# Kernel optimization log

Measured on AMD Instinct MI355X. Metric: run time of the kernel, lower is better.

The kernel has to match this reference:

```python
import jax, jax.numpy as jnp
import numpy as np

B, SEQ, D, H, E = 4, 4096, 1024, 4096, 8
CAPACITY = 2.0  # k = int(S * capacity) token-expert slots


def setup_inputs() -> dict:
    key = jax.random.key(0)
    ks = jax.random.split(key, 5)
    x = jax.random.normal(ks[0], (B, SEQ, D), dtype=jnp.float32)
    gate_weight = jax.random.normal(ks[1], (E, D), dtype=jnp.float32) * 0.006
    expert_bias = jnp.ones((E, 1), dtype=jnp.float32)
    W1 = jax.random.normal(ks[2], (E, D, H), dtype=jnp.float32) * 0.02
    b1 = jnp.zeros((E, H), dtype=jnp.float32)
    W2 = jax.random.normal(ks[3], (E, H, D), dtype=jnp.float32) * 0.02
    b2 = jnp.zeros((E, D), dtype=jnp.float32)
    return {"x": x, "gate_weight": gate_weight, "expert_bias": expert_bias,
            "W1": W1, "b1": b1, "W2": W2, "b2": b2}


def reference(x, gate_weight, expert_bias, W1, b1, W2, b2):
    Bv, s, Dv = x.shape
    xf = x.reshape(-1, Dv)               # [S, D]
    S = xf.shape[0]
    k = int(S * CAPACITY)

    # router: bias_sigmoid -> scores[e, s] = sigmoid(x @ gate.T + bias)
    logits = jnp.einsum('sd,ed->es', xf, gate_weight) + expert_bias  # [E, S]
    scores = jax.nn.sigmoid(logits)

    # global top-k over flattened (E*S) token-expert pairs
    value, index = jax.lax.top_k(scores.reshape(-1), k)
    index_expert = index // S
    index_token = index % S

    # combine weights: gating score at selected slots, 0 elsewhere (topk indices unique)
    C = jnp.zeros((E * S,), dtype=scores.dtype).at[index].set(value).reshape(E, S)

    token_each_expert = jax.ops.segment_sum(
        jnp.ones((k,), dtype=jnp.float32), index_expert, num_segments=E) / float(k)

    # per-expert MLP, gated combine (tokens with C==0 contribute exactly 0,
    # matching the torch gather/MLP/index_add_ path)
    out = jnp.zeros_like(xf)
    for e in range(E):
        h = jax.nn.gelu(xf @ W1[e] + b1[e], approximate=True)  # [S, H]
        y = h @ W2[e] + b2[e]                                  # [S, D]
        out = out + C[e][:, None] * y

    x_out = out.reshape(Bv, s, Dv)
    return x_out, token_each_expert, jnp.ones((E,), dtype=scores.dtype)
```

## Files before the change

### kernel.cpp

```cpp
#include <hip/hip_runtime.h>
#include <hip/hip_bf16.h>
#include <cstdint>
#include <cstdio>
#include <math.h>

#define S_TOK 16384
#define E_EXP 8
#define DDIM  1024
#define HDIM  4096
#define K_SEL 32768
#define ES    131072
#define OUT_XO 16777216

#define WS_META    0x000000u
#define WS_HIST    0x000100u
#define WS_COUNTS  0x001100u
#define WS_EXOFF   0x001200u
#define WS_TIEIDX  0x001300u
#define WS_CLEAR   0x00A000u
#define WS_TOK     0x010000u
#define WS_COEF    0x090000u
#define WS_SCORES  0x110000u
#define WS_TCNT    0x190000u
#define WS_TSLOT   0x1A0000u
#define WS_XB      0x400000u
#define WS_W1T    0x2400000u
#define WS_W2T    0x6400000u
#define WS_HBUF   0xA400000u
#define WS_TOTAL  0x1A400000u
#define WS_YBUF   WS_W1T

typedef __attribute__((ext_vector_type(4))) float f32x4;
typedef __attribute__((ext_vector_type(8))) short bf16x8;

__device__ __forceinline__ void gload_lds16(const void* g, void* l) {
  __builtin_amdgcn_global_load_lds((const __attribute__((address_space(1))) void*)g,
                                   (__attribute__((address_space(3))) void*)l, 16, 0, 0);
}

__device__ __forceinline__ float gelu_f(float x) {
  float u = __builtin_fmaf(x * x * x, 0.044715f, x);
  float e = __builtin_amdgcn_exp2f(-2.302207976f * u);
  return x * __builtin_amdgcn_rcpf(1.0f + e);
}

#define ABUF0 0
#define ABUF1 32768
#define BBUF0 65536
#define BBUF1 98304
#define HALF  16384

#define PH_BAR() __builtin_amdgcn_s_barrier()
#define SB0()    __builtin_amdgcn_sched_barrier(0)
#define LGK0()   do { asm volatile("s_waitcnt lgkmcnt(0)"); __builtin_amdgcn_sched_barrier(0); } while (0)
#define VMC6()   asm volatile("s_waitcnt vmcnt(6)")
#define VMC0()   asm volatile("s_waitcnt vmcnt(0)")

#define GLA(DSTOFF, KE, H) do { \
  gload_lds16(aS##H##0 + (KE), lds + (DSTOFF) + w * 2048); \
  gload_lds16(aS##H##1 + (KE), lds + (DSTOFF) + w * 2048 + 1024); } while (0)
#define GLB(DSTOFF, KE, H) do { \
  gload_lds16(bS##H##0 + (KE), lds + (DSTOFF) + w * 2048); \
  gload_lds16(bS##H##1 + (KE), lds + (DSTOFF) + w * 2048 + 1024); } while (0)

#define LOAD_A(AB, ILO) do { _Pragma("unroll") for (int ii = 0; ii < 4; ii++) { \
  aF[ii][0] = *(const bf16x8*)(lds + (AB) + arow + ((ILO) + ii) * 2048 + pc0); \
  aF[ii][1] = *(const bf16x8*)(lds + (AB) + arow + ((ILO) + ii) * 2048 + pc1); } } while (0)
#define LOAD_B(BB) do { _Pragma("unroll") for (int jj = 0; jj < 4; jj++) { \
  bF[jj][0] = *(const bf16x8*)(lds + (BB) + brow + jj * 2048 + pc0); \
  bF[jj][1] = *(const bf16x8*)(lds + (BB) + brow + jj * 2048 + pc1); } } while (0)

#define MFMA_Q(ILO, JLO) do { _Pragma("unroll") for (int ii = 0; ii < 4; ii++) \
  _Pragma("unroll") for (int jj = 0; jj < 2; jj++) { \
    acc[(ILO)+ii][(JLO)+jj] = __builtin_amdgcn_mfma_f32_16x16x32_bf16(aF[ii][0], bF[(JLO)+jj][0], acc[(ILO)+ii][(JLO)+jj], 0, 0, 0); \
    acc[(ILO)+ii][(JLO)+jj] = __builtin_amdgcn_mfma_f32_16x16x32_bf16(aF[ii][1], bF[(JLO)+jj][1], acc[(ILO)+ii][(JLO)+jj], 0, 0, 0); } } while (0)

#define KGROUP(K0, AB, BB, AO, P0STG, STG, ENDWAIT) do { \
  LOAD_A(AB, 0); LOAD_B(BB); \
  if (P0STG) { GLA((AO) + HALF, (K0) + 64, 1); } \
  PH_BAR(); LGK0(); \
  __builtin_amdgcn_s_setprio(1); MFMA_Q(0, 0); __builtin_amdgcn_s_setprio(0); \
  PH_BAR(); SB0(); \
  if (STG) { GLB((BB), (K0) + 128, 0); } \
  PH_BAR(); LGK0(); \
  __builtin_amdgcn_s_setprio(1); MFMA_Q(0, 2); __builtin_amdgcn_s_setprio(0); \
  PH_BAR(); SB0(); \
  LOAD_A(AB, 4); \
  if (STG) { GLB((BB) + HALF, (K0) + 128, 1); } \
  PH_BAR(); LGK0(); \
  __builtin_amdgcn_s_setprio(1); MFMA_Q(4, 2); __builtin_amdgcn_s_setprio(0); \
  PH_BAR(); SB0(); \
  if (STG) { GLA((AB), (K0) + 128, 0); } \
  PH_BAR(); LGK0(); \
  __builtin_amdgcn_s_setprio(1); MFMA_Q(4, 0); __builtin_amdgcn_s_setprio(0); \
  ENDWAIT; \
  PH_BAR(); SB0(); \
} while (0)

__global__ __launch_bounds__(256) void transpose_bf16_kernel(
    const float* __restrict__ in, __hip_bfloat16* __restrict__ outp, int R, int C)
{
  __shared__ float tile[32][33];
  const int c0 = blockIdx.x * 32, r0 = blockIdx.y * 32;
  const size_t eoff = (size_t)blockIdx.z * (size_t)R * (size_t)C;
  const float* ip = in + eoff;
  __hip_bfloat16* op = outp + eoff;
  const int tx = threadIdx.x, ty = threadIdx.y;
#pragma unroll
  for (int i = 0; i < 4; i++) {
    int r = ty + i * 8;
    tile[r][tx] = ip[(size_t)(r0 + r) * C + c0 + tx];
  }
  __syncthreads();
#pragma unroll
  for (int i = 0; i < 4; i++) {
    int c = ty + i * 8;
    op[(size_t)(c0 + c) * R + r0 + tx] = __float2bfloat16(tile[tx][c]);
  }
}

__global__ __launch_bounds__(256) void router_kernel(
    const float* __restrict__ x, const float* __restrict__ gw, const float* __restrict__ bias,
    float* __restrict__ scores, __hip_bfloat16* __restrict__ xb)
{
  __shared__ float g[E_EXP * DDIM];
  __shared__ float bs[E_EXP];
  const int tid = threadIdx.x;
  for (int i = tid; i < E_EXP * DDIM; i += 256) g[i] = gw[i];
  if (tid < E_EXP) bs[tid] = bias[tid];
  __syncthreads();
  const int w = tid >> 6, lane = tid & 63;
  const int s = blockIdx.x * 4 + w;
  double acc[E_EXP] = {0, 0, 0, 0, 0, 0, 0, 0};
  const float* xrow = x + (size_t)s * DDIM;
  __hip_bfloat16* xbrow = xb + (size_t)s * DDIM;
#pragma unroll 4
  for (int j = 0; j < 16; j++) {
    int d = lane + 64 * j;
    float xv = xrow[d];
    xbrow[d] = __float2bfloat16(xv);
#pragma unroll
    for (int e = 0; e < E_EXP; e++) acc[e] += (double)xv * (double)g[e * DDIM + d];
  }
#pragma unroll
  for (int e = 0; e < E_EXP; e++) {
    double a = acc[e];
#pragma unroll
    for (int off = 32; off > 0; off >>= 1) a += __shfl_xor(a, off);
    acc[e] = a;
  }
  if (lane == 0) {
#pragma unroll
    for (int e = 0; e < E_EXP; e++) {
      double lg = acc[e] + (double)bs[e];
      float sc = (float)(1.0 / (1.0 + exp(-lg)));
      scores[(size_t)e * S_TOK + s] = sc;
    }
  }
}

__global__ __launch_bounds__(256) void hist_pass_kernel(
    const float* __restrict__ scores, const unsigned* __restrict__ meta,
    unsigned* __restrict__ hist, int pass)
{
  __shared__ unsigned h[256];
  const int tid = threadIdx.x;
  h[tid] = 0;
  __syncthreads();
  const unsigned prefix = meta[0];
  const int pshift = 32 - 8 * pass;
  const int bshift = 24 - 8 * pass;
  const unsigned base = blockIdx.x * 2048 + tid;
#pragma unroll
  for (int i = 0; i < 8; i++) {
    unsigned b = __float_as_uint(scores[base + i * 256]);
    bool ok = (pass == 0) || ((b >> pshift) == prefix);
    if (ok) atomicAdd(&h[(b >> bshift) & 0xFFu], 1u);
  }
  __syncthreads();
  if (h[tid]) atomicAdd(&hist[tid], h[tid]);
}

__global__ __launch_bounds__(256) void scan_pass_kernel(
    const unsigned* __restrict__ hist, unsigned* __restrict__ meta, int final)
{
  const int t = threadIdx.x;
  const unsigned v = hist[t];
  const unsigned prefix = meta[0];
  const unsigned above = meta[1];
  __shared__ unsigned csum[256];
  csum[t] = v;
  __syncthreads();
  for (int off = 1; off < 256; off <<= 1) {
    unsigned add = (t + off < 256) ? csum[t + off] : 0u;
    __syncthreads();
    csum[t] += add;
    __syncthreads();
  }
  const unsigned cge = csum[t];
  const unsigned cgt = cge - v;
  if (above + cgt < K_SEL && above + cge >= K_SEL) {
    meta[0] = (prefix << 8) | (unsigned)t;
    meta[1] = above + cgt;
    if (final) {
      meta[2] = (prefix << 8) | (unsigned)t;
      meta[4] = K_SEL - (above + cgt);
    }
  }
}

__global__ __launch_bounds__(256) void sel_kernel(const float* __restrict__ scores,
                                                  unsigned* __restrict__ meta,
                                                  unsigned* __restrict__ counts,
                                                  int* __restrict__ tok_list,
                                                  float* __restrict__ coef_list,
                                                  unsigned* __restrict__ tie_idx,
                                                  unsigned* __restrict__ tcnt,
                                                  unsigned* __restrict__ tslot)
{
  __shared__ unsigned lcnt[E_EXP], lbase[E_EXP];
  const int tid = threadIdx.x;
  if (tid < E_EXP) lcnt[tid] = 0;
  __syncthreads();
  const unsigned i = blockIdx.x * 256 + tid;
  const float v = scores[i];
  const unsigned b = __float_as_uint(v);
  const unsigned t = meta[2];
  const bool sel = (b > t);
  const unsigned e = i >> 14;
  unsigned myslot = 0;
  if (sel) myslot = atomicAdd(&lcnt[e], 1u);
  else if (b == t) {
    unsigned ts = atomicAdd(&meta[5], 1u);
    if (ts < 8192u) tie_idx[ts] = i;
  }
  __syncthreads();
  if (tid < E_EXP) lbase[tid] = atomicAdd(&counts[tid], lcnt[tid]);
  __syncthreads();
  if (sel) {
    const unsigned slot = lbase[e] + myslot;
    const unsigned p = e * S_TOK + slot;
    const unsigned tok = i & 16383u;
    tok_list[p] = (int)tok;
    coef_list[p] = v;
    unsigned us = atomicAdd(&tcnt[tok], 1u);
    tslot[tok * 8u + us] = (e << 14) | slot;
  }
}

__global__ __launch_bounds__(256) void fin_kernel(const unsigned* __restrict__ meta,
                                                  const unsigned* __restrict__ tie_idx,
                                                  unsigned* __restrict__ counts,
                                                  int* __restrict__ tok_list,
                                                  float* __restrict__ coef_list,
                                                  unsigned* __restrict__ tcnt,
                                                  unsigned* __restrict__ tslot)
{
  unsigned tcnt_ties = meta[5]; if (tcnt_ties > 8192u) tcnt_ties = 8192u;
  const unsigned q = meta[4];
  const float tval = __uint_as_float(meta[2]);
  for (unsigned t = threadIdx.x; t < tcnt_ties; t += 256) {
    unsigned idx = tie_idx[t];
    unsigned rank = 0;
    for (unsigned u = 0; u < tcnt_ties; u++) rank += (tie_idx[u] < idx) ? 1u : 0u;
    if (rank < q) {
      const unsigned e = idx >> 14;
      const unsigned tok = idx & 16383u;
      const unsigned slot = atomicAdd(&counts[e], 1u);
      tok_list[e * S_TOK + slot] = (int)tok;
      coef_list[e * S_TOK + slot] = tval;
      unsigned us = atomicAdd(&tcnt[tok], 1u);
      tslot[tok * 8u + us] = (e << 14) | slot;
    }
  }
}

__global__ void tail_kernel(const unsigned* __restrict__ counts, unsigned* __restrict__ exoff,
                            float* __restrict__ tail)
{
  if (threadIdx.x == 0) {
    unsigned o = 0;
    for (int e = 0; e < E_EXP; e++) { exoff[e] = o; o += counts[e]; }
    exoff[E_EXP] = o;
  }
  if (threadIdx.x < E_EXP) {
    tail[threadIdx.x] = (float)counts[threadIdx.x] * (1.0f / (float)K_SEL);
    tail[E_EXP + threadIdx.x] = 1.0f;
  }
}

__global__ __launch_bounds__(512, 1) void gemm1_kernel(
    const __hip_bfloat16* __restrict__ xb,
    const __hip_bfloat16* __restrict__ w1t,
    const float* __restrict__ b1,
    const int* __restrict__ tok_list,
    const unsigned* __restrict__ counts,
    const unsigned* __restrict__ exoff,
    __hip_bfloat16* __restrict__ hbuf)
{
  const int e = blockIdx.z;
  const int cnt = (int)counts[e];
  const int m0 = blockIdx.y * 256;
  if (m0 >= cnt) return;
  const int n0 = blockIdx.x * 256;

  __shared__ __align__(16) char lds[131072];
  __shared__ int s_tok[256];

  const int tid = threadIdx.x;
  const int w = tid >> 6, lane = tid & 63;
  const int wm = w >> 2, wn = w & 3;

  if (tid < 256) {
    int mi = m0 + tid;
    s_tok[tid] = tok_list[e * S_TOK + (mi < cnt ? mi : cnt - 1)];
  }
  __syncthreads();

  const int srl0 = w * 16 + (lane >> 3);
  const int srl1 = srl0 + 8;
  const int gch = ((lane & 7) ^ (lane >> 3)) * 8;
  const __hip_bfloat16* aS00 = xb + (size_t)s_tok[srl0] * DDIM + gch;
  const __hip_bfloat16* aS01 = xb + (size_t)s_tok[srl1] * DDIM + gch;
  const __hip_bfloat16* aS10 = xb + (size_t)s_tok[128 + srl0] * DDIM + gch;
  const __hip_bfloat16* aS11 = xb + (size_t)s_tok[128 + srl1] * DDIM + gch;
  const __hip_bfloat16* w1e = w1t + (size_t)e * HDIM * DDIM;
  const __hip_bfloat16* bS00 = w1e + (size_t)(n0 + srl0) * DDIM + gch;
  const __hip_bfloat16* bS01 = w1e + (size_t)(n0 + srl1) * DDIM + gch;
  const __hip_bfloat16* bS10 = w1e + (size_t)(n0 + 128 + srl0) * DDIM + gch;
  const __hip_bfloat16* bS11 = w1e + (size_t)(n0 + 128 + srl1) * DDIM + gch;

  const int arow = (wm * 128 + (lane & 15)) * 128;
  const int brow = (wn * 64 + (lane & 15)) * 128;
  const int pc0 = (((lane >> 4)) ^ (lane & 7)) * 16;
  const int pc1 = (((lane >> 4) + 4) ^ (lane & 7)) * 16;

  f32x4 acc[8][4] = {};
  bf16x8 aF[4][2], bF[4][2];

  GLA(ABUF0, 0, 0); GLA(ABUF0 + HALF, 0, 1);
  GLB(BBUF0, 0, 0); GLB(BBUF0 + HALF, 0, 1);
  GLB(BBUF1, 64, 0); GLB(BBUF1 + HALF, 64, 1);
  GLA(ABUF1, 64, 0);
  VMC6(); PH_BAR(); SB0();

  const int NKT = DDIM / 64;
  int kt = 0;
  for (; kt + 2 < NKT; kt += 2) {
    KGROUP(kt * 64, ABUF0, BBUF0, ABUF1, true, true, VMC6());
    KGROUP((kt + 1) * 64, ABUF1, BBUF1, ABUF0, true, true, VMC6());
  }
  KGROUP(kt * 64, ABUF0, BBUF0, ABUF1, true, false, VMC0());
  KGROUP((kt + 1) * 64, ABUF1, BBUF1, ABUF0, false, false, );
  VMC0();
  __syncthreads();

  __hip_bfloat16* stg = (__hip_bfloat16*)lds;
  const float* b1e = b1 + (size_t)e * HDIM;
  float bvj[4];
#pragma unroll
  for (int j = 0; j < 4; j++) bvj[j] = b1e[n0 + wn * 64 + j * 16 + (lane & 15)];
  const int pbase = (int)exoff[e] + m0;

#pragma unroll
  for (int P = 0; P < 4; P++) {
    __syncthreads();
    if (wm == (P >> 1)) {
      const int ib = (P & 1) * 4;
#pragma unroll
      for (int ii = 0; ii < 4; ii++)
#pragma unroll
        for (int jj = 0; jj < 4; jj++)
#pragma unroll
          for (int r = 0; r < 4; r++) {
            const int rloc = ii * 16 + (lane >> 4) * 4 + r;
            const int col = wn * 64 + jj * 16 + (lane & 15);
            stg[rloc * 264 + col] = __float2bfloat16(gelu_f(acc[ib + ii][jj][r] + bvj[jj]));
          }
    }
    __syncthreads();
    const int rr = tid >> 3;
    const int m = P * 64 + rr;
    if (m0 + m < cnt) {
      __hip_bfloat16* dst = hbuf + (size_t)(pbase + m) * HDIM + n0;
      const __hip_bfloat16* src = stg + rr * 264;
#pragma unroll
      for (int c = 0; c < 4; c++)
        *(uint4*)(dst + (tid & 7) * 8 + c * 64) = *(const uint4*)(src + (tid & 7) * 8 + c * 64);
    }
  }
}

__global__ __launch_bounds__(512, 1) void gemm2_kernel(
    const __hip_bfloat16* __restrict__ hbuf,
    const __hip_bfloat16* __restrict__ w2t,
    const float* __restrict__ b2,
    const float* __restrict__ coef_list,
    const unsigned* __restrict__ counts,
    const unsigned* __restrict__ exoff,
    __hip_bfloat16* __restrict__ ybuf)
{
  const int e = blockIdx.z;
  const int cnt = (int)counts[e];
  const int m0 = blockIdx.y * 256;
  if (m0 >= cnt) return;
  const int n0 = blockIdx.x * 256;

  __shared__ __align__(16) char lds[131072];
  __shared__ float s_coef[256];

  const int tid = threadIdx.x;
  const int w = tid >> 6, lane = tid & 63;
  const int wm = w >> 2, wn = w & 3;
  const int pb = (int)exoff[e];

  if (tid < 256) {
    int mi = m0 + tid;
    s_coef[tid] = (mi < cnt) ? coef_list[e * S_TOK + mi] : 0.0f;
  }
  __syncthreads();

  const int srl0 = w * 16 + (lane >> 3);
  const int srl1 = srl0 + 8;
  const int gch = ((lane & 7) ^ (lane >> 3)) * 8;
  const int ra0 = pb + ((m0 + srl0 < cnt) ? m0 + srl0 : cnt - 1);
  const int ra1 = pb + ((m0 + srl1 < cnt) ? m0 + srl1 : cnt - 1);
  const int ra2 = pb + ((m0 + 128 + srl0 < cnt) ? m0 + 128 + srl0 : cnt - 1);
  const int ra3 = pb + ((m0 + 128 + srl1 < cnt) ? m0 + 128 + srl1 : cnt - 1);
  const __hip_bfloat16* aS00 = hbuf + (size_t)ra0 * HDIM + gch;
  const __hip_bfloat16* aS01 = hbuf + (size_t)ra1 * HDIM + gch;
  const __hip_bfloat16* aS10 = hbuf + (size_t)ra2 * HDIM + gch;
  const __hip_bfloat16* aS11 = hbuf + (size_t)ra3 * HDIM + gch;
  const __hip_bfloat16* w2e = w2t + (size_t)e * DDIM * HDIM;
  const __hip_bfloat16* bS00 = w2e + (size_t)(n0 + srl0) * HDIM + gch;
  const __hip_bfloat16* bS01 = w2e + (size_t)(n0 + srl1) * HDIM + gch;
  const __hip_bfloat16* bS10 = w2e + (size_t)(n0 + 128 + srl0) * HDIM + gch;
  const __hip_bfloat16* bS11 = w2e + (size_t)(n0 + 128 + srl1) * HDIM + gch;

  const int arow = (wm * 128 + (lane & 15)) * 128;
  const int brow = (wn * 64 + (lane & 15)) * 128;
  const int pc0 = (((lane >> 4)) ^ (lane & 7)) * 16;
  const int pc1 = (((lane >> 4) + 4) ^ (lane & 7)) * 16;

  f32x4 acc[8][4] = {};
  bf16x8 aF[4][2], bF[4][2];

  GLA(ABUF0, 0, 0); GLA(ABUF0 + HALF, 0, 1);
  GLB(BBUF0, 0, 0); GLB(BBUF0 + HALF, 0, 1);
  GLB(BBUF1, 64, 0); GLB(BBUF1 + HALF, 64, 1);
  GLA(ABUF1, 64, 0);
  VMC6(); PH_BAR(); SB0();

  const int NKT = HDIM / 64;
  int kt = 0;
  for (; kt + 2 < NKT; kt += 2) {
    KGROUP(kt * 64, ABUF0, BBUF0, ABUF1, true, true, VMC6());
    KGROUP((kt + 1) * 64, ABUF1, BBUF1, ABUF0, true, true, VMC6());
  }
  KGROUP(kt * 64, ABUF0, BBUF0, ABUF1, true, false, VMC0());
  KGROUP((kt + 1) * 64, ABUF1, BBUF1, ABUF0, false, false, );
  VMC0();
  __syncthreads();

  __hip_bfloat16* stg = (__hip_bfloat16*)lds;
  const float* b2e = b2 + (size_t)e * DDIM;
  float bvj[4];
#pragma unroll
  for (int j = 0; j < 4; j++) bvj[j] = b2e[n0 + wn * 64 + j * 16 + (lane & 15)];
  const int pbase = pb + m0;

#pragma unroll
  for (int P = 0; P < 4; P++) {
    __syncthreads();
    if (wm == (P >> 1)) {
      const int ib = (P & 1) * 4;
#pragma unroll
      for (int ii = 0; ii < 4; ii++)
#pragma unroll
        for (int jj = 0; jj < 4; jj++)
#pragma unroll
          for (int r = 0; r < 4; r++) {
            const int rloc = ii * 16 + (lane >> 4) * 4 + r;
            const int col = wn * 64 + jj * 16 + (lane & 15);
            const float cf = s_coef[P * 64 + rloc];
            stg[rloc * 264 + col] = __float2bfloat16(cf * (acc[ib + ii][jj][r] + bvj[jj]));
          }
    }
    __syncthreads();
    const int rr = tid >> 3;
    const int m = P * 64 + rr;
    if (m0 + m < cnt) {
      __hip_bfloat16* dst = ybuf + (size_t)(pbase + m) * DDIM + n0;
      const __hip_bfloat16* src = stg + rr * 264;
#pragma unroll
      for (int c = 0; c < 4; c++)
        *(uint4*)(dst + (tid & 7) * 8 + c * 64) = *(const uint4*)(src + (tid & 7) * 8 + c * 64);
    }
  }
}

__global__ __launch_bounds__(256) void combine_kernel(
    const __hip_bfloat16* __restrict__ ybuf,
    const unsigned* __restrict__ tcnt,
    const unsigned* __restrict__ tslot,
    const unsigned* __restrict__ exoff,
    float* __restrict__ out)
{
  const int tid = threadIdx.x;
  const int t = blockIdx.x * 2 + (tid >> 7);
  const int d0 = (tid & 127) * 8;
  float a[8] = {0, 0, 0, 0, 0, 0, 0, 0};
  const unsigned n = tcnt[t];
  for (unsigned s = 0; s < n; s++) {
    const unsigned code = tslot[t * 8u + s];
    const unsigned p = exoff[code >> 14] + (code & 16383u);
    bf16x8 v = *(const bf16x8*)(ybuf + (size_t)p * DDIM + d0);
#pragma unroll
    for (int k = 0; k < 8; k++)
      a[k] += __uint_as_float(((unsigned)(unsigned short)v[k]) << 16);
  }
  float* op = out + (size_t)t * DDIM + d0;
  *(float4*)op = make_float4(a[0], a[1], a[2], a[3]);
  *(float4*)(op + 4) = make_float4(a[4], a[5], a[6], a[7]);
}

extern "C" void kernel_launch(void* const* d_in, const int* in_sizes, int n_in,
                              void* d_out, int out_size, void* d_ws, size_t ws_size,
                              hipStream_t stream) {
  const float* x    = (const float*)d_in[0];
  const float* gw   = (const float*)d_in[1];
  const float* bias = (const float*)d_in[2];
  const float* W1   = (const float*)d_in[3];
  const float* b1   = (const float*)d_in[4];
  const float* W2   = (const float*)d_in[5];
  const float* b2   = (const float*)d_in[6];
  float* out = (float*)d_out;
  char* ws = (char*)d_ws;

  if (ws_size < (size_t)WS_TOTAL) {
    fprintf(stderr, "kernel_launch: ws_size %zu < required %u\n", ws_size, WS_TOTAL);
    return;
  }

  unsigned* meta   = (unsigned*)(ws + WS_META);
  unsigned* hist   = (unsigned*)(ws + WS_HIST);
  unsigned* counts = (unsigned*)(ws + WS_COUNTS);
  unsigned* exoff  = (unsigned*)(ws + WS_EXOFF);
  unsigned* tiei   = (unsigned*)(ws + WS_TIEIDX);
  unsigned* tcnt   = (unsigned*)(ws + WS_TCNT);
  unsigned* tslot  = (unsigned*)(ws + WS_TSLOT);
  int*      tokl   = (int*)(ws + WS_TOK);
  float*    coefl  = (float*)(ws + WS_COEF);
  float*    scores = (float*)(ws + WS_SCORES);
  __hip_bfloat16* xb   = (__hip_bfloat16*)(ws + WS_XB);
  __hip_bfloat16* w1t  = (__hip_bfloat16*)(ws + WS_W1T);
  __hip_bfloat16* w2t  = (__hip_bfloat16*)(ws + WS_W2T);
  __hip_bfloat16* hbuf = (__hip_bfloat16*)(ws + WS_HBUF);
  __hip_bfloat16* ybuf = (__hip_bfloat16*)(ws + WS_YBUF);

  hipMemsetAsync(ws, 0, WS_CLEAR, stream);
  hipMemsetAsync(ws + WS_TCNT, 0, S_TOK * sizeof(unsigned), stream);

  transpose_bf16_kernel<<<dim3(HDIM / 32, DDIM / 32, E_EXP), dim3(32, 8), 0, stream>>>(W1, w1t, DDIM, HDIM);
  transpose_bf16_kernel<<<dim3(DDIM / 32, HDIM / 32, E_EXP), dim3(32, 8), 0, stream>>>(W2, w2t, HDIM, DDIM);

  router_kernel<<<S_TOK / 4, 256, 0, stream>>>(x, gw, bias, scores, xb);

  for (int p = 0; p < 4; p++) {
    hist_pass_kernel<<<ES / 2048, 256, 0, stream>>>(scores, meta, hist + p * 256, p);
    scan_pass_kernel<<<1, 256, 0, stream>>>(hist + p * 256, meta, p == 3);
  }
  sel_kernel<<<ES / 256, 256, 0, stream>>>(scores, meta, counts, tokl, coefl, tiei, tcnt, tslot);
  fin_kernel<<<1, 256, 0, stream>>>(meta, tiei, counts, tokl, coefl, tcnt, tslot);
  tail_kernel<<<1, 64, 0, stream>>>(counts, exoff, out + OUT_XO);

  gemm1_kernel<<<dim3(HDIM / 256, S_TOK / 256, E_EXP), 512, 0, stream>>>(
      xb, w1t, b1, tokl, counts, exoff, hbuf);
  gemm2_kernel<<<dim3(DDIM / 256, S_TOK / 256, E_EXP), 512, 0, stream>>>(
      hbuf, w2t, b2, coefl, counts, exoff, ybuf);
  combine_kernel<<<S_TOK / 2, 256, 0, stream>>>(ybuf, tcnt, tslot, exoff, out);
}
```

Measured before the change: 954.7 us.

## Restructure GEMM main loop into two-phase tiles with register-prefetched B fragments

Replaces the four-phase KGROUP schedule, which had many barriers and lgkmcnt waits, with a two-barrier-per-tile schedule in both expert GEMM kernels. A fragments are split into a03/a47 halves and B fragments into b01/b23 halves. The next tile's B fragments are read from LDS while the current MFMAs run, and global-to-LDS staging for A and B is issued at whole-tile granularity. The aim is fewer barriers and better overlap of LDS reads with MFMA work. In exchange, each tile now waits for vmcnt(0) instead of leaving loads in flight, and register pressure rises.

```diff
diff --git a/kernel.cpp b/kernel.cpp
--- a/kernel.cpp
+++ b/kernel.cpp
@@ -51,50 +51,59 @@
 #define HALF  16384
 
 #define PH_BAR() __builtin_amdgcn_s_barrier()
-#define SB0()    __builtin_amdgcn_sched_barrier(0)
-#define LGK0()   do { asm volatile("s_waitcnt lgkmcnt(0)"); __builtin_amdgcn_sched_barrier(0); } while (0)
-#define VMC6()   asm volatile("s_waitcnt vmcnt(6)")
-#define VMC0()   asm volatile("s_waitcnt vmcnt(0)")
-
-#define GLA(DSTOFF, KE, H) do { \
-  gload_lds16(aS##H##0 + (KE), lds + (DSTOFF) + w * 2048); \
-  gload_lds16(aS##H##1 + (KE), lds + (DSTOFF) + w * 2048 + 1024); } while (0)
-#define GLB(DSTOFF, KE, H) do { \
-  gload_lds16(bS##H##0 + (KE), lds + (DSTOFF) + w * 2048); \
-  gload_lds16(bS##H##1 + (KE), lds + (DSTOFF) + w * 2048 + 1024); } while (0)
-
-#define LOAD_A(AB, ILO) do { _Pragma("unroll") for (int ii = 0; ii < 4; ii++) { \
-  aF[ii][0] = *(const bf16x8*)(lds + (AB) + arow + ((ILO) + ii) * 2048 + pc0); \
-  aF[ii][1] = *(const bf16x8*)(lds + (AB) + arow + ((ILO) + ii) * 2048 + pc1); } } while (0)
-#define LOAD_B(BB) do { _Pragma("unroll") for (int jj = 0; jj < 4; jj++) { \
-  bF[jj][0] = *(const bf16x8*)(lds + (BB) + brow + jj * 2048 + pc0); \
-  bF[jj][1] = *(const bf16x8*)(lds + (BB) + brow + jj * 2048 + pc1); } } while (0)
-
-#define MFMA_Q(ILO, JLO) do { _Pragma("unroll") for (int ii = 0; ii < 4; ii++) \
+#define VMC0M()  asm volatile("s_waitcnt vmcnt(0)" ::: "memory")
+
+#define STAGE_A(DST, KE) do { \
+  gload_lds16(aS00 + (KE), lds + (DST) + w * 2048); \
+  gload_lds16(aS01 + (KE), lds + (DST) + w * 2048 + 1024); \
+  gload_lds16(aS10 + (KE), lds + (DST) + HALF + w * 2048); \
+  gload_lds16(aS11 + (KE), lds + (DST) + HALF + w * 2048 + 1024); } while (0)
+#define STAGE_B(DST, KE) do { \
+  gload_lds16(bS00 + (KE), lds + (DST) + w * 2048); \
+  gload_lds16(bS01 + (KE), lds + (DST) + w * 2048 + 1024); \
+  gload_lds16(bS10 + (KE), lds + (DST) + HALF + w * 2048); \
+  gload_lds16(bS11 + (KE), lds + (DST) + HALF + w * 2048 + 1024); } while (0)
+
+#define LDS_A03(AB) { _Pragma("unroll") for (int ii = 0; ii < 4; ii++) { \
+  a03[ii][0] = *(const bf16x8*)(lds + (AB) + arow + ii * 2048 + pc0); \
+  a03[ii][1] = *(const bf16x8*)(lds + (AB) + arow + ii * 2048 + pc1); } }
+#define LDS_A47(AB) { _Pragma("unroll") for (int ii = 0; ii < 4; ii++) { \
+  a47[ii][0] = *(const bf16x8*)(lds + (AB) + arow + (4 + ii) * 2048 + pc0); \
+  a47[ii][1] = *(const bf16x8*)(lds + (AB) + arow + (4 + ii) * 2048 + pc1); } }
+#define LDS_B01(BB) { _Pragma("unroll") for (int jj = 0; jj < 2; jj++) { \
+  b01[jj][0] = *(const bf16x8*)(lds + (BB) + brow + jj * 2048 + pc0); \
+  b01[jj][1] = *(const bf16x8*)(lds + (BB) + brow + jj * 2048 + pc1); } }
+#define LDS_B23(BB) { _Pragma("unroll") for (int jj = 0; jj < 2; jj++) { \
+  b23[jj][0] = *(const bf16x8*)(lds + (BB) + brow + (2 + jj) * 2048 + pc0); \
+  b23[jj][1] = *(const bf16x8*)(lds + (BB) + brow + (2 + jj) * 2048 + pc1); } }
+
+#define MF(AA, BF, IL, JL) { _Pragma("unroll") for (int ii = 0; ii < 4; ii++) \
   _Pragma("unroll") for (int jj = 0; jj < 2; jj++) { \
-    acc[(ILO)+ii][(JLO)+jj] = __builtin_amdgcn_mfma_f32_16x16x32_bf16(aF[ii][0], bF[(JLO)+jj][0], acc[(ILO)+ii][(JLO)+jj], 0, 0, 0); \
-    acc[(ILO)+ii][(JLO)+jj] = __builtin_amdgcn_mfma_f32_16x16x32_bf16(aF[ii][1], bF[(JLO)+jj][1], acc[(ILO)+ii][(JLO)+jj], 0, 0, 0); } } while (0)
-
-#define KGROUP(K0, AB, BB, AO, P0STG, STG, ENDWAIT) do { \
-  LOAD_A(AB, 0); LOAD_B(BB); \
-  if (P0STG) { GLA((AO) + HALF, (K0) + 64, 1); } \
-  PH_BAR(); LGK0(); \
-  __builtin_amdgcn_s_setprio(1); MFMA_Q(0, 0); __builtin_amdgcn_s_setprio(0); \
-  PH_BAR(); SB0(); \
-  if (STG) { GLB((BB), (K0) + 128, 0); } \
-  PH_BAR(); LGK0(); \
-  __builtin_amdgcn_s_setprio(1); MFMA_Q(0, 2); __builtin_amdgcn_s_setprio(0); \
-  PH_BAR(); SB0(); \
-  LOAD_A(AB, 4); \
-  if (STG) { GLB((BB) + HALF, (K0) + 128, 1); } \
-  PH_BAR(); LGK0(); \
-  __builtin_amdgcn_s_setprio(1); MFMA_Q(4, 2); __builtin_amdgcn_s_setprio(0); \
-  PH_BAR(); SB0(); \
-  if (STG) { GLA((AB), (K0) + 128, 0); } \
-  PH_BAR(); LGK0(); \
-  __builtin_amdgcn_s_setprio(1); MFMA_Q(4, 0); __builtin_amdgcn_s_setprio(0); \
-  ENDWAIT; \
-  PH_BAR(); SB0(); \
+    acc[(IL)+ii][(JL)+jj] = __builtin_amdgcn_mfma_f32_16x16x32_bf16(AA[ii][0], BF[jj][0], acc[(IL)+ii][(JL)+jj], 0, 0, 0); \
+    acc[(IL)+ii][(JL)+jj] = __builtin_amdgcn_mfma_f32_16x16x32_bf16(AA[ii][1], BF[jj][1], acc[(IL)+ii][(JL)+jj], 0, 0, 0); } }
+
+#define TILE(T, AB, BB, ABn, BBn, STGA, STGB) do { \
+  PH_BAR(); \
+  LDS_A03(AB); \
+  if (STGA) STAGE_A(ABn, ((T) + 1) * 64); \
+  __builtin_amdgcn_s_setprio(1); MF(a03, b01, 0, 0); MF(a03, b23, 0, 2); __builtin_amdgcn_s_setprio(0); \
+  VMC0M(); \
+  PH_BAR(); \
+  LDS_A47(AB); \
+  if (STGB) STAGE_B(BB, ((T) + 2) * 64); \
+  __builtin_amdgcn_s_setprio(1); MF(a47, b01, 4, 0); __builtin_amdgcn_s_setprio(0); \
+  LDS_B01(BBn); \
+  __builtin_amdgcn_s_setprio(1); MF(a47, b23, 4, 2); __builtin_amdgcn_s_setprio(0); \
+  LDS_B23(BBn); \
+} while (0)
+
+#define TILE_LAST(AB, BB) do { \
+  PH_BAR(); \
+  LDS_A03(AB); \
+  __builtin_amdgcn_s_setprio(1); MF(a03, b01, 0, 0); MF(a03, b23, 0, 2); __builtin_amdgcn_s_setprio(0); \
+  PH_BAR(); \
+  LDS_A47(AB); \
+  __builtin_amdgcn_s_setprio(1); MF(a47, b01, 4, 0); MF(a47, b23, 4, 2); __builtin_amdgcn_s_setprio(0); \
 } while (0)
 
 __global__ __launch_bounds__(256) void transpose_bf16_kernel(
@@ -336,23 +345,23 @@
   const int pc1 = (((lane >> 4) + 4) ^ (lane & 7)) * 16;
 
   f32x4 acc[8][4] = {};
-  bf16x8 aF[4][2], bF[4][2];
-
-  GLA(ABUF0, 0, 0); GLA(ABUF0 + HALF, 0, 1);
-  GLB(BBUF0, 0, 0); GLB(BBUF0 + HALF, 0, 1);
-  GLB(BBUF1, 64, 0); GLB(BBUF1 + HALF, 64, 1);
-  GLA(ABUF1, 64, 0);
-  VMC6(); PH_BAR(); SB0();
+  bf16x8 a03[4][2], a47[4][2], b01[2][2], b23[2][2];
+
+  STAGE_A(ABUF0, 0);
+  STAGE_B(BBUF0, 0);
+  STAGE_B(BBUF1, 64);
+  VMC0M();
+  PH_BAR();
+  LDS_B01(BBUF0); LDS_B23(BBUF0);
 
   const int NKT = DDIM / 64;
   int kt = 0;
   for (; kt + 2 < NKT; kt += 2) {
-    KGROUP(kt * 64, ABUF0, BBUF0, ABUF1, true, true, VMC6());
-    KGROUP((kt + 1) * 64, ABUF1, BBUF1, ABUF0, true, true, VMC6());
-  }
-  KGROUP(kt * 64, ABUF0, BBUF0, ABUF1, true, false, VMC0());
-  KGROUP((kt + 1) * 64, ABUF1, BBUF1, ABUF0, false, false, );
-  VMC0();
+    TILE(kt,     ABUF0, BBUF0, ABUF1, BBUF1, true, true);
+    TILE(kt + 1, ABUF1, BBUF1, ABUF0, BBUF0, true, true);
+  }
+  TILE(kt, ABUF0, BBUF0, ABUF1, BBUF1, true, false);
+  TILE_LAST(ABUF1, BBUF1);
   __syncthreads();
 
   __hip_bfloat16* stg = (__hip_bfloat16*)lds;
@@ -443,23 +452,23 @@
   const int pc1 = (((lane >> 4) + 4) ^ (lane & 7)) * 16;
 
   f32x4 acc[8][4] = {};
-  bf16x8 aF[4][2], bF[4][2];
-
-  GLA(ABUF0, 0, 0); GLA(ABUF0 + HALF, 0, 1);
-  GLB(BBUF0, 0, 0); GLB(BBUF0 + HALF, 0, 1);
-  GLB(BBUF1, 64, 0); GLB(BBUF1 + HALF, 64, 1);
-  GLA(ABUF1, 64, 0);
-  VMC6(); PH_BAR(); SB0();
+  bf16x8 a03[4][2], a47[4][2], b01[2][2], b23[2][2];
+
+  STAGE_A(ABUF0, 0);
+  STAGE_B(BBUF0, 0);
+  STAGE_B(BBUF1, 64);
+  VMC0M();
+  PH_BAR();
+  LDS_B01(BBUF0); LDS_B23(BBUF0);
 
   const int NKT = HDIM / 64;
   int kt = 0;
   for (; kt + 2 < NKT; kt += 2) {
-    KGROUP(kt * 64, ABUF0, BBUF0, ABUF1, true, true, VMC6());
-    KGROUP((kt + 1) * 64, ABUF1, BBUF1, ABUF0, true, true, VMC6());
-  }
-  KGROUP(kt * 64, ABUF0, BBUF0, ABUF1, true, false, VMC0());
-  KGROUP((kt + 1) * 64, ABUF1, BBUF1, ABUF0, false, false, );
-  VMC0();
+    TILE(kt,     ABUF0, BBUF0, ABUF1, BBUF1, true, true);
+    TILE(kt + 1, ABUF1, BBUF1, ABUF0, BBUF0, true, true);
+  }
+  TILE(kt, ABUF0, BBUF0, ABUF1, BBUF1, true, false);
+  TILE_LAST(ABUF1, BBUF1);
   __syncthreads();
 
   __hip_bfloat16* stg = (__hip_bfloat16*)lds;
```

New measurement: 947.0 us. About the same (-0.8%).
